# Kernel optimization log

Measured on AMD Instinct MI355X. Metric: run time of the kernel, lower is better.

The kernel has to match this reference:

```python
import jax, jax.numpy as jnp
import numpy as np

B, S, D, H = 64, 65536, 512, 256
H2 = H // 2
CAP_LIMIT = 0.85
ACT_THR = 0.5


def _normalize(x):
    return x / jnp.maximum(jnp.linalg.norm(x, axis=-1, keepdims=True), 1e-12)


def _layernorm(x, g, b):
    m = x.mean(-1, keepdims=True)
    v = ((x - m) ** 2).mean(-1, keepdims=True)
    return (x - m) / jnp.sqrt(v + 1e-5) * g + b


def setup_inputs() -> dict:
    key = jax.random.key(0)
    ks = jax.random.split(key, 20)

    def lin(k, i, o):
        s = 1.0 / np.sqrt(i)
        kw, kb = jax.random.split(k)
        return (jax.random.uniform(kw, (i, o), minval=-s, maxval=s),
                jax.random.uniform(kb, (o,), minval=-s, maxval=s))

    inp = {}
    inp["new_content"] = jax.random.normal(ks[0], (B, D), dtype=jnp.float32)
    inp["query"] = jax.random.normal(ks[1], (B, D), dtype=jnp.float32)
    inp["memory_bank"] = jax.random.normal(ks[2], (S, D), dtype=jnp.float32)
    inp["access_times"] = jax.random.uniform(ks[3], (S,), minval=0.0, maxval=900.0)
    inp["current_step"] = 1000
    inp["sr_w1"], inp["sr_b1"] = lin(ks[4], 2 * D, H)
    inp["sr_g"] = jnp.ones((H,), jnp.float32)
    inp["sr_beta"] = jnp.zeros((H,), jnp.float32)
    inp["sr_w2"], inp["sr_b2"] = lin(ks[5], H, H2)
    inp["sn_w"], inp["sn_b"] = lin(ks[6], D, H2)
    inp["sg_w"], inp["sg_b"] = lin(ks[7], H2, 1)
    inp["el_w"], inp["el_b"] = lin(ks[8], 1, 32)
    inp["ec_w"], inp["ec_b"] = lin(ks[9], D, 32)
    inp["eg_w"], inp["eg_b"] = lin(ks[10], 64, 1)
    inp["dd_w1"], inp["dd_b1"] = lin(ks[11], 2 * D, H)
    inp["dd_w2"], inp["dd_b2"] = lin(ks[12], H, 1)
    inp["ds_w1"], inp["ds_b1"] = lin(ks[13], 2 * D, H)
    inp["ds_w2"], inp["ds_b2"] = lin(ks[14], H, 1)
    return inp


def _forward(new_content, query, memory_bank, access_times,
             sr_w1, sr_b1, sr_g, sr_beta, sr_w2, sr_b2,
             sn_w, sn_b, sg_w, sg_b,
             el_w, el_b, ec_w, ec_b, eg_w, eg_b,
             dd_w1, dd_b1, dd_w2, dd_b2,
             ds_w1, ds_b1, ds_w2, ds_b2,
             step):
    mem = memory_bank
    at = access_times
    norms = jnp.linalg.norm(mem, axis=-1)               # [S]
    capacity = jnp.mean((norms > ACT_THR).astype(jnp.float32))
    dyn_thr = jnp.clip(
        jnp.where(capacity < 0.3, 0.08,
                  jnp.where(capacity < 0.6, 0.08 + (capacity - 0.3) * 0.733,
                            0.3 + (capacity - 0.6))), 0.0, 0.7)
    topk_thr = jnp.where(capacity < 0.3, 0.1, jnp.where(capacity < 0.6, 0.2, 0.4))
    raw_thr = jnp.where(capacity < 0.3, 0.3, 0.5)

    # store relevance / novelty / gate
    combined = jnp.concatenate([new_content, query], -1)          # [B,2D]
    h = _layernorm(combined @ sr_w1 + sr_b1, sr_g, sr_beta)
    rel = jax.nn.relu(jax.nn.relu(h) @ sr_w2 + sr_b2)             # [B,H2]
    nn_ = _normalize(new_content)
    sims = nn_ @ _normalize(mem).T                                # [B,S]
    max_sim = sims.max(-1, keepdims=True)
    novelty = (1.0 - max_sim) / 2.0                               # [B,1]
    nf = jax.nn.sigmoid(new_content @ sn_w + sn_b)
    store_score = jax.nn.sigmoid((rel + nf) @ sg_w + sg_b)        # [B,1]

    # novelty percentile over active slots (no boolean-shape gather)
    active = norms > ACT_THR
    n_active = active.sum()
    nov_mean = novelty.mean()
    cond = (nov_mean > (1.0 - sims)) & active[None, :]
    denom = (new_content.shape[0] * jnp.maximum(n_active, 1)).astype(jnp.float32)
    perc = jnp.where(n_active > 0, cond.sum().astype(jnp.float32) / denom, 1.0)

    base_store = store_score.mean() > raw_thr
    novelty_ok = nov_mean > dyn_thr
    topk_ok = perc > topk_thr
    should_store = base_store & novelty_ok & topk_ok

    # emergency erase (capacity over limit)
    do_erase = capacity > CAP_LIMIT
    age = jnp.maximum(step - at, 0.0)
    es_em = age / (age.max() + 1e-6) + (1.0 - jax.nn.sigmoid(norms))
    victim = jnp.argmax(es_em)
    mem = jnp.where(do_erase, mem.at[victim].set(0.0), mem)
    at = jnp.where(do_erase, at.at[victim].set(-99999.0), at)
    should_store = should_store & jnp.logical_not(do_erase & jnp.logical_not(novelty_ok))

    # per-slot erase scores
    lru = jax.nn.relu(((step - at) / 1000.0)[:, None] @ el_w + el_b)   # [S,32]
    conf = jax.nn.sigmoid(mem @ ec_w + ec_b)                            # [S,32]
    erase_scores = jax.nn.sigmoid(jnp.concatenate([lru, conf], -1) @ eg_w + eg_b)[:, 0]

    # conflict detection: top-3 similar slots, gather-MLP-scatter drift
    sims2 = _normalize(new_content) @ _normalize(mem).T                # [B,S]
    tv, ti = jax.lax.top_k(sims2, 3)                                   # [B,3]
    cmask = (tv > 0.7) & (tv < 0.99)
    gathered = mem[ti]                                                 # [B,3,D]
    pair = jnp.concatenate([jnp.broadcast_to(new_content[:, None, :], gathered.shape), gathered], -1)
    prob = jax.nn.sigmoid(jax.nn.relu(pair @ dd_w1 + dd_b1) @ dd_w2 + dd_b2)[..., 0]
    strength = jax.nn.sigmoid(jax.nn.relu(pair @ ds_w1 + ds_b1) @ ds_w2 + ds_b2)[..., 0]
    apply_m = cmask & (prob > 0.5)                                     # [B,3]
    avg = (new_content[:, None, :] + gathered) / 2.0
    s = strength[..., None]
    dn_cand = (1.0 - s) * new_content[:, None, :] + s * avg
    do_cand = (1.0 - s) * gathered + s * avg
    drifted_new = new_content
    for k in range(3):  # fixed k=3, later k overwrites (matches torch inner loop)
        drifted_new = jnp.where(apply_m[:, k:k + 1], dn_cand[:, k], drifted_new)
    for k in range(3):
        idx = ti[:, k]
        cur = mem[idx]
        mem = mem.at[idx].set(jnp.where(apply_m[:, k, None], do_cand[:, k], cur))

    # conditional write
    slot_age = step - at
    recent = (at >= 0.0) & (slot_age < 3.0)
    masked = erase_scores * (~recent).astype(erase_scores.dtype)
    masked = jnp.where(masked.max() <= 0.0, slot_age, masked)
    write_idx = jnp.where(do_erase, victim, jnp.argmax(masked))
    erase_out = jnp.where(should_store & jnp.logical_not(do_erase), masked, erase_scores)
    mem = jnp.where(should_store, mem.at[write_idx].set(drifted_new[0]), mem)
    at = jnp.where(should_store, at.at[write_idx].set(step), at)

    recent_changes = jnp.abs(mem - memory_bank).mean()
    return (mem, at, erase_out, store_score[:, 0], novelty[:, 0], recent_changes)


def reference(new_content, query, memory_bank, access_times,
              sr_w1, sr_b1, sr_g, sr_beta, sr_w2, sr_b2,
              sn_w, sn_b, sg_w, sg_b,
              el_w, el_b, ec_w, ec_b, eg_w, eg_b,
              dd_w1, dd_b1, dd_w2, dd_b2,
              ds_w1, ds_b1, ds_w2, ds_b2,
              current_step):
    step = jnp.float32(current_step)
    return _forward(new_content, query, memory_bank, access_times,
                    sr_w1, sr_b1, sr_g, sr_beta, sr_w2, sr_b2,
                    sn_w, sn_b, sg_w, sg_b,
                    el_w, el_b, ec_w, ec_b, eg_w, eg_b,
                    dd_w1, dd_b1, dd_w2, dd_b2,
                    ds_w1, ds_b1, ds_w2, ds_b2, step)
```

## Files before the change

kernel.cpp:

```cpp
#include <hip/hip_runtime.h>
#include <math.h>
#include <limits.h>

#define S_N 65536
#define D_N 512
#define B_N 64

typedef __attribute__((ext_vector_type(8))) short short8;
typedef __attribute__((ext_vector_type(4))) float f32x4;

#define SIMS_F      (B_N*S_N/2)
#define OFF_SIMS    0
#define OFF_AEXT    (OFF_SIMS + SIMS_F)
#define AEXT_F      (96*512/2)
#define OFF_NORMS   (OFF_AEXT + AEXT_F)
#define OFF_CONF    (OFF_NORMS + S_N)
#define OFF_FLAGS   (OFF_CONF + S_N)
#define OFF_LIST    (OFF_FLAGS + S_N)
#define OFF_MASKED  (OFF_LIST + 256)
#define OFF_ERSC    (OFF_MASKED + S_N)
#define OFF_SLOTAGE (OFF_ERSC + S_N)
#define OFF_STORES  (OFF_SLOTAGE + S_N)
#define OFF_MAXSIM  (OFF_STORES + 64)
#define OFF_TI      (OFF_MAXSIM + 64)
#define OFF_TV      (OFF_TI + 192)
#define OFF_APPLY   (OFF_TV + 192)
#define OFF_HM      (OFF_APPLY + 192)
#define OFF_HNC     (OFF_HM + 32768)
#define OFF_HG      (OFF_HNC + 65536)
#define OFF_DNC0    (OFF_HG + 196608)
#define OFF_DRIFT0  (OFF_DNC0 + 1536)
#define OFF_DOCAND  (OFF_DRIFT0 + 512)
#define OFF_SCAL    (OFF_DOCAND + 98304)

#define OUT_MEM 0
#define OUT_AT  (S_N*D_N)
#define OUT_ER  (OUT_AT + S_N)
#define OUT_SS  (OUT_ER + S_N)
#define OUT_NOV (OUT_SS + 64)
#define OUT_RC  (OUT_NOV + 64)

struct __align__(8) Scal {
  unsigned long long victim_pack;
  unsigned long long masked_pack;
  unsigned long long slotage_pack;
  int cnt_active;
  int cond_cnt;
  unsigned age_max_t;
  float nov_mean;
  float changed_sum;
  int do_erase;
  int should_store;
  int write_idx;
  int victim_idx;
  int list_cnt;
};

__device__ __forceinline__ float sigmoidf_(float x){ return 1.0f/(1.0f+expf(-x)); }
__device__ __forceinline__ unsigned f2mono(float f){
  unsigned u = __float_as_uint(f);
  return (u & 0x80000000u) ? ~u : (u | 0x80000000u);
}
__device__ __forceinline__ float mono2f(unsigned m){
  unsigned u = (m & 0x80000000u) ? (m & 0x7FFFFFFFu) : ~m;
  return __uint_as_float(u);
}
__device__ __forceinline__ unsigned long long packvi(float v, int i){
  return (((unsigned long long)f2mono(v)) << 32) | (unsigned long long)(0xFFFFFFFFu - (unsigned)i);
}
__device__ __forceinline__ bool betterVI(float v, int i, float v2, int i2){
  return (v > v2) || (v == v2 && i < i2);
}
__device__ __forceinline__ unsigned short bf16r(float f){
  unsigned u = __float_as_uint(f);
  return (unsigned short)((u + 0x7fffu + ((u>>16)&1u)) >> 16);
}
__device__ __forceinline__ float bf2f(unsigned short h){
  return __uint_as_float(((unsigned)h)<<16);
}
__device__ __forceinline__ void touch_row(int row, float* ws){
  int* flags = (int*)(ws + OFF_FLAGS);
  if (atomicExch(&flags[row], 1) == 0){
    Scal* sc = (Scal*)(ws + OFF_SCAL);
    int i = atomicAdd(&sc->list_cnt, 1);
    ((int*)(ws + OFF_LIST))[i] = row;
  }
}

__device__ __forceinline__ void gld16(const float* g, void* l){
  __builtin_amdgcn_global_load_lds((const __attribute__((address_space(1))) void*)g,
                                   (__attribute__((address_space(3))) void*)l, 16, 0, 0);
}
#define WAITV(N) asm volatile("s_waitcnt vmcnt(" #N ")" ::: "memory")

__global__ __launch_bounds__(256) void k_initm(const float* __restrict__ nc,
                                               const float* __restrict__ qr,
                                               const float* __restrict__ at_in,
                                               const float* __restrict__ ec_w,
                                               const int* __restrict__ step_p,
                                               const float* __restrict__ sr_w1,
                                               float* __restrict__ ws, float* __restrict__ out){
  int blk = blockIdx.x, t = threadIdx.x;
  Scal* sc = (Scal*)(ws + OFF_SCAL);
  unsigned short* aB = (unsigned short*)(ws + OFF_AEXT);
  __shared__ float red[256];
  __shared__ float ch[512];
  if (blk == 0){
    if (t == 0){
      sc->victim_pack = 0ULL; sc->masked_pack = 0ULL; sc->slotage_pack = 0ULL;
      sc->cnt_active = 0; sc->cond_cnt = 0; sc->age_max_t = 0u;
      sc->nov_mean = 0.0f; sc->changed_sum = 0.0f;
      sc->do_erase = 0; sc->should_store = 0; sc->write_idx = 0; sc->victim_idx = 0;
      sc->list_cnt = 0;
      out[OUT_RC] = 0.0f;
    }
    if (t < 64) ((unsigned*)(ws + OFF_MAXSIM))[t] = 0u;
  } else if (blk <= 64){
    int b = blk - 1;
    float x0 = nc[b*512 + t], x1 = nc[b*512 + 256 + t];
    red[t] = x0*x0 + x1*x1;
    __syncthreads();
    for (int o=128;o>0;o>>=1){ if (t<o) red[t]+=red[t+o]; __syncthreads(); }
    float inv = 1.0f / fmaxf(sqrtf(red[0]), 1e-12f);
    aB[b*512 + t]       = bf16r(x0*inv);
    aB[b*512 + 256 + t] = bf16r(x1*inv);
  } else if (blk <= 96){
    int j = blk - 65;
    for (int d=t; d<512; d+=256) aB[(64+j)*512 + d] = bf16r(ec_w[d*32 + j]);
  } else if (blk <= 160){
    int part = blk - 97;
    float stepf = (float)step_p[0];
    float lmaxv = -1e30f;
    for (int s = part*1024 + t; s < (part+1)*1024; s += 256)
      lmaxv = fmaxf(lmaxv, fmaxf(stepf - at_in[s], 0.0f));
    red[t]=lmaxv; __syncthreads();
    for (int o=128;o>0;o>>=1){ if (t<o) red[t]=fmaxf(red[t],red[t+o]); __syncthreads(); }
    if (t==0) atomicMax(&sc->age_max_t, f2mono(red[0]));
  } else if (blk <= 224){
    int part = blk - 161;
    for (int s = part*1024 + t; s < (part+1)*1024; s += 256)
      out[OUT_AT + s] = at_in[s];
  } else if (blk <= 288){
    int part = blk - 225;
    int* flags = (int*)(ws + OFF_FLAGS);
    for (int s = part*1024 + t; s < (part+1)*1024; s += 256) flags[s] = 0;
  } else {
    int blk2 = blk - 289;
    int b = blk2 >> 1, half = blk2 & 1;
    const float* src = half ? qr : nc;
    ch[t] = src[b*512 + t]; ch[256+t] = src[b*512 + 256 + t];
    __syncthreads();
    float h = 0.f;
    const float* w = sr_w1 + (half*512)*256 + t;
    for (int i=0;i<512;i++) h = fmaf(ch[i], w[i*256], h);
    ws[OFF_HM + (half*64 + b)*256 + t] = h;
  }
}

__global__ __launch_bounds__(256) void k_phase1(const float* __restrict__ mem,
                                                const float* __restrict__ ec_b,
                                                const float* __restrict__ eg_w,
                                                float* __restrict__ ws, float* __restrict__ out){
  __shared__ __align__(16) unsigned short aT[96*520];
  __shared__ __align__(16) char chunks[4*4*2048];
  __shared__ unsigned lmax[64];
  int t = threadIdx.x;
  int s0 = blockIdx.x * 64;
  Scal* sc = (Scal*)(ws + OFF_SCAL);
  int lane = t & 63, wv = t >> 6;
  int quad = lane >> 4, l15 = lane & 15;
  int row = wv*16 + l15;

  {
    const uint4* src = (const uint4*)(ws + OFF_AEXT);
    #pragma unroll
    for (int i=0;i<24;i++){
      int idx = i*256 + t;
      int arow = idx >> 6, c16 = idx & 63;
      uint4 v = src[idx];
      *(uint4*)((char*)aT + arow*1040 + c16*16) = v;
    }
    if (t < 64) lmax[t] = 0u;
  }
  __syncthreads();

  const float* gsrc = mem + ((size_t)(s0 + row))*512 + quad*8;
  float* od = out + OUT_MEM + ((size_t)(s0 + row))*512 + quad*8;
  char* mybuf = chunks + wv*8192;
  #define STAGE(c) do{ \
    gld16(gsrc + (c)*32,     mybuf + ((c)&3)*2048); \
    gld16(gsrc + (c)*32 + 4, mybuf + ((c)&3)*2048 + 1024); \
  }while(0)

  STAGE(0); asm volatile("" ::: "memory");
  STAGE(1); asm volatile("" ::: "memory");
  STAGE(2); asm volatile("" ::: "memory");

  f32x4 acc[6];
  #pragma unroll
  for (int r=0;r<6;r++) acc[r] = (f32x4){0.f,0.f,0.f,0.f};
  float ssq = 0.f;

  #pragma unroll
  for (int c=0;c<16;c++){
    if (c < 13) STAGE(c+3);
    if      (c == 0)  WAITV(6);
    else if (c == 1)  WAITV(8);
    else if (c == 2)  WAITV(10);
    else if (c <= 12) WAITV(12);
    else if (c == 13) WAITV(10);
    else if (c == 14) WAITV(8);
    else              WAITV(6);
    __builtin_amdgcn_sched_barrier(0);
    const char* bp = mybuf + (c&3)*2048;
    float4 v0 = *(const float4*)(bp + lane*16);
    float4 v1 = *(const float4*)(bp + 1024 + lane*16);
    *(float4*)(od + c*32)     = v0;
    *(float4*)(od + c*32 + 4) = v1;
    ssq = fmaf(v0.x,v0.x,ssq); ssq = fmaf(v0.y,v0.y,ssq);
    ssq = fmaf(v0.z,v0.z,ssq); ssq = fmaf(v0.w,v0.w,ssq);
    ssq = fmaf(v1.x,v1.x,ssq); ssq = fmaf(v1.y,v1.y,ssq);
    ssq = fmaf(v1.z,v1.z,ssq); ssq = fmaf(v1.w,v1.w,ssq);
    short8 bfrag;
    bfrag[0]=(short)bf16r(v0.x); bfrag[1]=(short)bf16r(v0.y);
    bfrag[2]=(short)bf16r(v0.z); bfrag[3]=(short)bf16r(v0.w);
    bfrag[4]=(short)bf16r(v1.x); bfrag[5]=(short)bf16r(v1.y);
    bfrag[6]=(short)bf16r(v1.z); bfrag[7]=(short)bf16r(v1.w);
    #pragma unroll
    for (int rt=0;rt<6;rt++){
      short8 afrag = *(const short8*)&aT[(rt*16 + l15)*520 + c*32 + quad*8];
      acc[rt] = __builtin_amdgcn_mfma_f32_16x16x32_bf16(afrag, bfrag, acc[rt], 0,0,0);
    }
  }
  #undef STAGE

  ssq += __shfl_xor(ssq, 16);
  ssq += __shfl_xor(ssq, 32);
  float nrm = sqrtf(ssq);
  float lv = 1.0f / fmaxf(nrm, 1e-12f);
  if (quad == 0) ws[OFF_NORMS + s0 + row] = nrm;
  unsigned long long m = __ballot(quad==0 && nrm > 0.5f);
  if (lane == 0) atomicAdd(&sc->cnt_active, (int)__popcll(m));

  unsigned short* simsb = (unsigned short*)(ws + OFF_SIMS);
  #pragma unroll
  for (int rt=0;rt<4;rt++){
    #pragma unroll
    for (int r=0;r<4;r++){
      int a = rt*16 + quad*4 + r;
      float sim = acc[rt][r] * lv;
      simsb[(size_t)a*S_N + s0 + row] = bf16r(sim);
      atomicMax(&lmax[a], f2mono(sim));
    }
  }
  float cpart = 0.f;
  #pragma unroll
  for (int rt=4;rt<6;rt++){
    #pragma unroll
    for (int r=0;r<4;r++){
      int j = (rt-4)*16 + quad*4 + r;
      cpart += sigmoidf_(acc[rt][r] + ec_b[j]) * eg_w[32+j];
    }
  }
  cpart += __shfl_down(cpart, 32);
  cpart += __shfl_down(cpart, 16);
  if (lane < 16) ws[OFF_CONF + s0 + row] = cpart;
  __syncthreads();
  if (t < 64) atomicMax(((unsigned*)(ws + OFF_MAXSIM)) + t, lmax[t]);
}

__global__ __launch_bounds__(256) void k_victim(const float* __restrict__ at_in,
                                                const int* __restrict__ step_p,
                                                float* __restrict__ ws){
  int t = threadIdx.x;
  Scal* sc = (Scal*)(ws + OFF_SCAL);
  float stepf = (float)step_p[0];
  float agemax = mono2f(sc->age_max_t);
  const float* norms = ws + OFF_NORMS;
  int gid = blockIdx.x*256 + t;
  int gstride = gridDim.x*256;
  unsigned long long best = 0ULL;
  for (int s = gid; s < S_N; s += gstride){
    float age = fmaxf(stepf - at_in[s], 0.0f);
    float es = age/(agemax + 1e-6f) + (1.0f - sigmoidf_(norms[s]));
    unsigned long long pk = packvi(es, s);
    if (pk > best) best = pk;
  }
  __shared__ unsigned long long redp[256];
  redp[t] = best; __syncthreads();
  for (int o=128;o>0;o>>=1){
    if (t<o && redp[t+o] > redp[t]) redp[t] = redp[t+o];
    __syncthreads();
  }
  if (t == 0) atomicMax(&sc->victim_pack, redp[0]);
}

__global__ __launch_bounds__(256) void k_mid(const float* __restrict__ nc, const float* __restrict__ qr,
    const float* __restrict__ sr_b1, const float* __restrict__ sr_g, const float* __restrict__ sr_beta,
    const float* __restrict__ sr_w2, const float* __restrict__ sr_b2,
    const float* __restrict__ sn_w,  const float* __restrict__ sn_b,
    const float* __restrict__ sg_w,  const float* __restrict__ sg_b,
    const float* __restrict__ ec_b,  const float* __restrict__ eg_w,
    float* __restrict__ ws, float* __restrict__ out){
  int blk = blockIdx.x, t = threadIdx.x;
  Scal* sc = (Scal*)(ws + OFF_SCAL);
  __shared__ float red[256];
  __shared__ float comb[1024];
  __shared__ float hbuf[256];
  __shared__ float sv[256*3];
  __shared__ int   si[256*3];

  if (blk == 64){
    const unsigned* gms = (const unsigned*)(ws + OFF_MAXSIM);
    float nv = 0.0f;
    if (t < 64){
      float msim = mono2f(gms[t]);
      nv = (1.0f - msim) * 0.5f;
      out[OUT_NOV + t] = nv;
    }
    red[t] = (t < 64) ? nv : 0.0f;
    __syncthreads();
    for (int o=128;o>0;o>>=1){ if (t<o) red[t]+=red[t+o]; __syncthreads(); }
    if (t == 0) sc->nov_mean = red[0] / 64.0f;
    return;
  }
  if (blk < 64){
    int b = blk;
    comb[t]       = nc[b*512 + t];
    comb[256 + t] = nc[b*512 + 256 + t];
    comb[512 + t] = qr[b*512 + t];
    comb[768 + t] = qr[b*512 + 256 + t];
    float h = ws[OFF_HM + b*256 + t] + ws[OFF_HM + (64 + b)*256 + t] + sr_b1[t];
    red[t] = h; __syncthreads();
    for (int o=128;o>0;o>>=1){ if (t<o) red[t]+=red[t+o]; __syncthreads(); }
    float mean = red[0] / 256.0f;
    __syncthreads();
    float dx = h - mean;
    red[t] = dx*dx; __syncthreads();
    for (int o=128;o>0;o>>=1){ if (t<o) red[t]+=red[t+o]; __syncthreads(); }
    float var = red[0] / 256.0f;
    __syncthreads();
    float hn = dx / sqrtf(var + 1e-5f) * sr_g[t] + sr_beta[t];
    hbuf[t] = fmaxf(hn, 0.0f);
    __syncthreads();
    float val = 0.0f;
    if (t < 128){
      float r = sr_b2[t];
      for (int j=0;j<256;j++) r = fmaf(hbuf[j], sr_w2[j*128 + t], r);
      r = fmaxf(r, 0.0f);
      float nf = sn_b[t];
      for (int d=0; d<512; d++) nf = fmaf(comb[d], sn_w[d*128 + t], nf);
      nf = sigmoidf_(nf);
      val = (r + nf) * sg_w[t];
    }
    red[t] = val; __syncthreads();
    for (int o=128;o>0;o>>=1){ if (t<o) red[t]+=red[t+o]; __syncthreads(); }
    if (t == 0){
      float ssc = sigmoidf_(red[0] + sg_b[0]);
      out[OUT_SS + b] = ssc;
      ws[OFF_STORES + b] = ssc;
    }
    return;
  }
  if (blk == 65){
    float capacity = (float)sc->cnt_active / 65536.0f;
    int de = (capacity > 0.85f) ? 1 : 0;
    int victim = (int)(0xFFFFFFFFu - (unsigned)(sc->victim_pack & 0xFFFFFFFFULL));
    if (t == 0){ sc->do_erase = de; sc->victim_idx = victim; }
    if (de){
      for (int d=t; d<512; d+=256) out[OUT_MEM + victim*512 + d] = 0.0f;
      if (t == 0){
        out[OUT_AT + victim] = -99999.0f;
        touch_row(victim, ws);
        float sum = 0.0f;
        for (int j=0;j<32;j++) sum += sigmoidf_(ec_b[j]) * eg_w[32 + j];
        ws[OFF_CONF + victim] = sum;
      }
    }
    return;
  }
  if (blk < 578){
    const unsigned* gms = (const unsigned*)(ws + OFF_MAXSIM);
    red[t] = (t < 64) ? (1.0f - mono2f(gms[t])) * 0.5f : 0.0f;
    __syncthreads();
    for (int o=128;o>0;o>>=1){ if (t<o) red[t]+=red[t+o]; __syncthreads(); }
    float thr = 1.0f - red[0] / 64.0f;
    const unsigned* simsu = (const unsigned*)(ws + OFF_SIMS);
    const float* norms = ws + OFF_NORMS;
    int gid = (blk - 66)*256 + t;
    int gstride = 512*256;
    int cnt = 0;
    for (int idx = gid; idx < B_N*S_N/2; idx += gstride){
      unsigned u = simsu[idx];
      int s = (idx*2) & (S_N-1);
      float v0 = __uint_as_float(u<<16);
      float v1 = __uint_as_float(u & 0xffff0000u);
      if (v0 > thr && norms[s]   > 0.5f) cnt++;
      if (v1 > thr && norms[s+1] > 0.5f) cnt++;
    }
    __syncthreads();
    int* redc = (int*)red;
    redc[t] = cnt;
    __syncthreads();
    for (int o=128;o>0;o>>=1){ if (t<o) redc[t]+=redc[t+o]; __syncthreads(); }
    if (t == 0) atomicAdd(&sc->cond_cnt, redc[0]);
    return;
  }
  {
    int b = blk - 578;
    int victim = (int)(0xFFFFFFFFu - (unsigned)(sc->victim_pack & 0xFFFFFFFFULL));
    int de = (((float)sc->cnt_active / 65536.0f) > 0.85f) ? 1 : 0;
    const unsigned short* simrow = (const unsigned short*)(ws + OFF_SIMS) + (size_t)b*S_N;
    float v[3] = {-1e30f,-1e30f,-1e30f};
    int ix[3] = {INT_MAX, INT_MAX, INT_MAX};
    for (int s = t; s < S_N; s += 256){
      float val = bf2f(simrow[s]);
      if (de && s == victim) val = 0.0f;
      if (betterVI(val, s, v[2], ix[2])){
        if (betterVI(val, s, v[1], ix[1])){
          if (betterVI(val, s, v[0], ix[0])){
            v[2]=v[1]; ix[2]=ix[1]; v[1]=v[0]; ix[1]=ix[0]; v[0]=val; ix[0]=s;
          } else { v[2]=v[1]; ix[2]=ix[1]; v[1]=val; ix[1]=s; }
        } else { v[2]=val; ix[2]=s; }
      }
    }
    for (int r=0;r<3;r++){ sv[t*3+r]=v[r]; si[t*3+r]=ix[r]; }
    for (int off=128; off>0; off>>=1){
      __syncthreads();
      if (t < off){
        float av[3], bv[3], ov[3]; int ai[3], bi[3], oi[3];
        for (int r=0;r<3;r++){ av[r]=sv[t*3+r]; ai[r]=si[t*3+r]; bv[r]=sv[(t+off)*3+r]; bi[r]=si[(t+off)*3+r]; }
        int ap=0, bp=0;
        for (int r=0;r<3;r++){
          bool takeA = (bp>=3) || (ap<3 && betterVI(av[ap],ai[ap],bv[bp],bi[bp]));
          if (takeA){ ov[r]=av[ap]; oi[r]=ai[ap]; ap++; }
          else      { ov[r]=bv[bp]; oi[r]=bi[bp]; bp++; }
        }
        for (int r=0;r<3;r++){ sv[t*3+r]=ov[r]; si[t*3+r]=oi[r]; }
      }
    }
    __syncthreads();
    if (t == 0){
      for (int k=0;k<3;k++){
        ws[OFF_TV + b*3 + k] = sv[k];
        ((int*)(ws + OFF_TI))[b*3 + k] = si[k];
      }
    }
  }
}

__global__ __launch_bounds__(256) void k_mlp2(const float* __restrict__ nc,
    const float* __restrict__ dd_w1, const float* __restrict__ ds_w1,
    float* __restrict__ ws, float* __restrict__ out){
  int blk = blockIdx.x, t = threadIdx.x;
  int b = blk >> 2, ks = blk & 3;
  __shared__ float ch[3*256];
  if (ks < 2){
    ch[t] = nc[b*512 + ks*256 + t];
    __syncthreads();
    float hd = 0.f, hs = 0.f;
    const float* wd = dd_w1 + (ks*256)*256 + t;
    const float* wq = ds_w1 + (ks*256)*256 + t;
    for (int i=0;i<256;i++){
      float c = ch[i];
      hd = fmaf(c, wd[i*256], hd);
      hs = fmaf(c, wq[i*256], hs);
    }
    float* H = ws + OFF_HNC + ((ks*64 + b)*2)*256;
    H[t] = hd; H[256 + t] = hs;
  } else {
    int ks2 = ks - 2;
    const int* tip = (const int*)(ws + OFF_TI);
    int r0 = tip[b*3], r1 = tip[b*3+1], r2 = tip[b*3+2];
    ch[t]       = out[OUT_MEM + (size_t)r0*512 + ks2*256 + t];
    ch[256 + t] = out[OUT_MEM + (size_t)r1*512 + ks2*256 + t];
    ch[512 + t] = out[OUT_MEM + (size_t)r2*512 + ks2*256 + t];
    __syncthreads();
    float hd0=0,hd1=0,hd2=0,hs0=0,hs1=0,hs2=0;
    const float* wd = dd_w1 + (512 + ks2*256)*256 + t;
    const float* wq = ds_w1 + (512 + ks2*256)*256 + t;
    for (int i=0;i<256;i++){
      float w0 = wd[i*256], w1 = wq[i*256];
      float c0 = ch[i], c1 = ch[256+i], c2 = ch[512+i];
      hd0=fmaf(c0,w0,hd0); hd1=fmaf(c1,w0,hd1); hd2=fmaf(c2,w0,hd2);
      hs0=fmaf(c0,w1,hs0); hs1=fmaf(c1,w1,hs1); hs2=fmaf(c2,w1,hs2);
    }
    float* H = ws + OFF_HG;
    int p0 = b*3;
    H[((ks2*192 + p0+0)*2+0)*256 + t] = hd0;
    H[((ks2*192 + p0+1)*2+0)*256 + t] = hd1;
    H[((ks2*192 + p0+2)*2+0)*256 + t] = hd2;
    H[((ks2*192 + p0+0)*2+1)*256 + t] = hs0;
    H[((ks2*192 + p0+1)*2+1)*256 + t] = hs1;
    H[((ks2*192 + p0+2)*2+1)*256 + t] = hs2;
  }
}

__global__ __launch_bounds__(256) void k_pairfin(const float* __restrict__ nc,
    const float* __restrict__ dd_b1, const float* __restrict__ dd_w2, const float* __restrict__ dd_b2,
    const float* __restrict__ ds_b1, const float* __restrict__ ds_w2, const float* __restrict__ ds_b2,
    float* __restrict__ ws, float* __restrict__ out){
  int p = blockIdx.x, t = threadIdx.x;
  int b = p / 3, k = p - 3*b;
  const int* tip = (const int*)(ws + OFF_TI);
  int row = tip[p];
  float hd = ws[OFF_HNC + ((0*64+b)*2+0)*256 + t] + ws[OFF_HNC + ((1*64+b)*2+0)*256 + t]
           + ws[OFF_HG + ((0*192+p)*2+0)*256 + t] + ws[OFF_HG + ((1*192+p)*2+0)*256 + t] + dd_b1[t];
  float hs = ws[OFF_HNC + ((0*64+b)*2+1)*256 + t] + ws[OFF_HNC + ((1*64+b)*2+1)*256 + t]
           + ws[OFF_HG + ((0*192+p)*2+1)*256 + t] + ws[OFF_HG + ((1*192+p)*2+1)*256 + t] + ds_b1[t];
  __shared__ float red[256];
  __shared__ float bc[2];
  red[t] = fmaxf(hd, 0.f) * dd_w2[t];
  __syncthreads();
  for (int o=128;o>0;o>>=1){ if (t<o) red[t]+=red[t+o]; __syncthreads(); }
  if (t == 0) bc[0] = red[0] + dd_b2[0];
  __syncthreads();
  red[t] = fmaxf(hs, 0.f) * ds_w2[t];
  __syncthreads();
  for (int o=128;o>0;o>>=1){ if (t<o) red[t]+=red[t+o]; __syncthreads(); }
  if (t == 0) bc[1] = red[0] + ds_b2[0];
  __syncthreads();
  float prob  = sigmoidf_(bc[0]);
  float stren = sigmoidf_(bc[1]);
  float tvv = ws[OFF_TV + p];
  int ap = (tvv > 0.7f && tvv < 0.99f && prob > 0.5f) ? 1 : 0;
  if (t == 0){
    ((int*)(ws + OFF_APPLY))[p] = ap;
    touch_row(row, ws);
  }
  for (int d=t; d<512; d+=256){
    float n = nc[b*512 + d];
    float g = out[OUT_MEM + (size_t)row*512 + d];
    float avg = 0.5f*(n + g);
    ws[OFF_DOCAND + p*512 + d] = (1.0f - stren)*g + stren*avg;
    if (b == 0) ws[OFF_DNC0 + k*512 + d] = (1.0f - stren)*n + stren*avg;
  }
}

__global__ __launch_bounds__(256) void k_scer(const int* __restrict__ step_p,
    const float* __restrict__ el_w, const float* __restrict__ el_b,
    const float* __restrict__ eg_w, const float* __restrict__ eg_b,
    float* __restrict__ ws, float* __restrict__ out){
  int blk = blockIdx.x, t = threadIdx.x;
  Scal* sc = (Scal*)(ws + OFF_SCAL);
  __shared__ unsigned long long rm[256], rs[256];
  if (blk < 2){
    int d = blk*256 + t;
    const int* tip = (const int*)(ws + OFF_TI);
    const int* ap  = (const int*)(ws + OFF_APPLY);
    for (int k=0;k<3;k++){
      float cur[64];
      #pragma unroll
      for (int b=0;b<64;b++) cur[b] = out[OUT_MEM + (size_t)tip[b*3 + k]*512 + d];
      #pragma unroll
      for (int b=0;b<64;b++){
        int p = b*3 + k;
        float v = ap[p] ? ws[OFF_DOCAND + p*512 + d] : cur[b];
        out[OUT_MEM + (size_t)tip[p]*512 + d] = v;
      }
    }
    return;
  }
  float stepf = (float)step_p[0];
  float egb = eg_b[0];
  int gid = (blk-2)*256 + t;
  int gstride = 64*256;
  unsigned long long bm = 0ULL, bs = 0ULL;
  for (int s = gid; s < S_N; s += gstride){
    float a = out[OUT_AT + s];
    float x = (stepf - a) / 1000.0f;
    float lp = 0.0f;
    #pragma unroll
    for (int j=0;j<32;j++) lp += fmaxf(x*el_w[j] + el_b[j], 0.0f) * eg_w[j];
    float er = sigmoidf_(lp + ws[OFF_CONF + s] + egb);
    float sa = stepf - a;
    bool recent = (a >= 0.0f) && (sa < 3.0f);
    float msk = recent ? 0.0f : er;
    ws[OFF_ERSC + s] = er;
    ws[OFF_MASKED + s] = msk;
    ws[OFF_SLOTAGE + s] = sa;
    unsigned long long pm = packvi(msk, s); if (pm > bm) bm = pm;
    unsigned long long ps = packvi(sa,  s); if (ps > bs) bs = ps;
  }
  rm[t]=bm; rs[t]=bs; __syncthreads();
  for (int o=128;o>0;o>>=1){
    if (t<o){ if (rm[t+o]>rm[t]) rm[t]=rm[t+o]; if (rs[t+o]>rs[t]) rs[t]=rs[t+o]; }
    __syncthreads();
  }
  if (t == 0){
    atomicMax(&sc->masked_pack, rm[0]);
    atomicMax(&sc->slotage_pack, rs[0]);
  }
}

__global__ __launch_bounds__(256) void k_finalout(const float* __restrict__ nc,
                                                  const int* __restrict__ step_p,
                                                  float* __restrict__ ws, float* __restrict__ out){
  int blk = blockIdx.x, t = threadIdx.x;
  Scal* sc = (Scal*)(ws + OFF_SCAL);
  __shared__ float red[64];
  __shared__ int sh_ss, sh_wi;
  if (t < 64) red[t] = ws[OFF_STORES + t];
  __syncthreads();
  for (int o=32;o>0;o>>=1){ if (t<o) red[t]+=red[t+o]; __syncthreads(); }
  if (t == 0){
    float store_mean = red[0] / 64.0f;
    int cnt = sc->cnt_active;
    float capacity = (float)cnt / 65536.0f;
    float dyn_thr;
    if (capacity < 0.3f) dyn_thr = 0.08f;
    else if (capacity < 0.6f) dyn_thr = 0.08f + (capacity - 0.3f)*0.733f;
    else dyn_thr = 0.3f + (capacity - 0.6f);
    dyn_thr = fminf(fmaxf(dyn_thr, 0.0f), 0.7f);
    float topk_thr = (capacity < 0.3f) ? 0.1f : ((capacity < 0.6f) ? 0.2f : 0.4f);
    float raw_thr  = (capacity < 0.3f) ? 0.3f : 0.5f;
    int base_store = store_mean > raw_thr;
    int novelty_ok = sc->nov_mean > dyn_thr;
    int cmax = cnt > 1 ? cnt : 1;
    float denom = (float)(64 * cmax);
    float perc = (cnt > 0) ? ((float)sc->cond_cnt) / denom : 1.0f;
    int topk_ok = perc > topk_thr;
    int de = sc->do_erase;
    int ss = base_store && novelty_ok && topk_ok;
    if (de && !novelty_ok) ss = 0;
    float mmax = mono2f((unsigned)(sc->masked_pack >> 32));
    int marg = (int)(0xFFFFFFFFu - (unsigned)(sc->masked_pack  & 0xFFFFFFFFULL));
    int sarg = (int)(0xFFFFFFFFu - (unsigned)(sc->slotage_pack & 0xFFFFFFFFULL));
    sh_ss = ss;
    sh_wi = de ? sc->victim_idx : ((mmax > 0.0f) ? marg : sarg);
  }
  __syncthreads();
  int ss = sh_ss, de = sc->do_erase;
  if (blk == 64){
    if (ss){
      int wi = sh_wi;
      const int* ap = (const int*)(ws + OFF_APPLY);
      for (int d=t; d<512; d+=256){
        float v = nc[d];
        if (ap[0]) v = ws[OFF_DNC0 + 0*512 + d];
        if (ap[1]) v = ws[OFF_DNC0 + 1*512 + d];
        if (ap[2]) v = ws[OFF_DNC0 + 2*512 + d];
        out[OUT_MEM + (size_t)wi*512 + d] = v;
      }
      if (t == 0){
        out[OUT_AT + wi] = (float)step_p[0];
        touch_row(wi, ws);
      }
    }
    return;
  }
  float mmax = mono2f((unsigned)(sc->masked_pack >> 32));
  bool usemask = ss && !de;
  for (int s = blk*256 + t; s < S_N; s += 64*256){
    float v;
    if (usemask) v = (mmax <= 0.0f) ? ws[OFF_SLOTAGE + s] : ws[OFF_MASKED + s];
    else v = ws[OFF_ERSC + s];
    out[OUT_ER + s] = v;
  }
}

__global__ __launch_bounds__(256) void k_diff(const float* __restrict__ mem,
                                              float* __restrict__ ws, float* __restrict__ out){
  int t = threadIdx.x;
  Scal* sc = (Scal*)(ws + OFF_SCAL);
  int cnt = sc->list_cnt;
  const int* list = (const int*)(ws + OFF_LIST);
  float lsum = 0.0f;
  for (int i = blockIdx.x; i < cnt; i += gridDim.x){
    int row = list[i];
    float part = 0.0f;
    for (int d=t; d<512; d+=256)
      part += fabsf(out[OUT_MEM + (size_t)row*512 + d] - mem[(size_t)row*512 + d]);
    lsum += part;
  }
  __shared__ float red[256];
  red[t] = lsum; __syncthreads();
  for (int o=128;o>0;o>>=1){ if (t<o) red[t]+=red[t+o]; __syncthreads(); }
  if (t == 0 && red[0] != 0.0f) atomicAdd(out + OUT_RC, red[0] * (1.0f/33554432.0f));
}

extern "C" void kernel_launch(void* const* d_in, const int* in_sizes, int n_in,
                              void* d_out, int out_size, void* d_ws, size_t ws_size,
                              hipStream_t stream) {
  const float* nc    = (const float*)d_in[0];
  const float* qr    = (const float*)d_in[1];
  const float* mem   = (const float*)d_in[2];
  const float* at    = (const float*)d_in[3];
  const int*   step  = (const int*)  d_in[4];
  const float* sr_w1 = (const float*)d_in[5];
  const float* sr_b1 = (const float*)d_in[6];
  const float* sr_g  = (const float*)d_in[7];
  const float* sr_be = (const float*)d_in[8];
  const float* sr_w2 = (const float*)d_in[9];
  const float* sr_b2 = (const float*)d_in[10];
  const float* sn_w  = (const float*)d_in[11];
  const float* sn_b  = (const float*)d_in[12];
  const float* sg_w  = (const float*)d_in[13];
  const float* sg_b  = (const float*)d_in[14];
  const float* el_w  = (const float*)d_in[15];
  const float* el_b  = (const float*)d_in[16];
  const float* ec_w  = (const float*)d_in[17];
  const float* ec_b  = (const float*)d_in[18];
  const float* eg_w  = (const float*)d_in[19];
  const float* eg_b  = (const float*)d_in[20];
  const float* dd_w1 = (const float*)d_in[21];
  const float* dd_b1 = (const float*)d_in[22];
  const float* dd_w2 = (const float*)d_in[23];
  const float* dd_b2 = (const float*)d_in[24];
  const float* ds_w1 = (const float*)d_in[25];
  const float* ds_b1 = (const float*)d_in[26];
  const float* ds_w2 = (const float*)d_in[27];
  const float* ds_b2 = (const float*)d_in[28];
  float* out = (float*)d_out;
  float* ws  = (float*)d_ws;

  k_initm    <<<dim3(417), dim3(256), 0, stream>>>(nc, qr, at, ec_w, step, sr_w1, ws, out);
  k_phase1   <<<dim3(1024), dim3(256), 0, stream>>>(mem, ec_b, eg_w, ws, out);
  k_victim   <<<dim3(64), dim3(256), 0, stream>>>(at, step, ws);
  k_mid      <<<dim3(642), dim3(256), 0, stream>>>(nc, qr, sr_b1, sr_g, sr_be,
                                                   sr_w2, sr_b2, sn_w, sn_b, sg_w, sg_b,
                                                   ec_b, eg_w, ws, out);
  k_mlp2     <<<dim3(256), dim3(256), 0, stream>>>(nc, dd_w1, ds_w1, ws, out);
  k_pairfin  <<<dim3(192), dim3(256), 0, stream>>>(nc, dd_b1, dd_w2, dd_b2,
                                                   ds_b1, ds_w2, ds_b2, ws, out);
  k_scer     <<<dim3(66), dim3(256), 0, stream>>>(step, el_w, el_b, eg_w, eg_b, ws, out);
  k_finalout <<<dim3(65), dim3(256), 0, stream>>>(nc, step, ws, out);
  k_diff     <<<dim3(64), dim3(256), 0, stream>>>(mem, ws, out);
}
```

Before: 502.6 us.

## Split small MLP matvecs across more blocks with K-split partial sums

```diff
diff --git a/kernel.cpp b/kernel.cpp
--- a/kernel.cpp
+++ b/kernel.cpp
@@ -31,6 +31,7 @@
 #define OFF_DNC0    (OFF_HG + 196608)
 #define OFF_DRIFT0  (OFF_DNC0 + 1536)
 #define OFF_DOCAND  (OFF_DRIFT0 + 512)
+#define OFF_SNP     OFF_DOCAND
 #define OFF_SCAL    (OFF_DOCAND + 98304)
 
 #define OUT_MEM 0
@@ -99,12 +100,13 @@
                                                const float* __restrict__ ec_w,
                                                const int* __restrict__ step_p,
                                                const float* __restrict__ sr_w1,
+                                               const float* __restrict__ sn_w,
                                                float* __restrict__ ws, float* __restrict__ out){
   int blk = blockIdx.x, t = threadIdx.x;
   Scal* sc = (Scal*)(ws + OFF_SCAL);
   unsigned short* aB = (unsigned short*)(ws + OFF_AEXT);
   __shared__ float red[256];
-  __shared__ float ch[512];
+  __shared__ float ch[256];
   if (blk == 0){
     if (t == 0){
       sc->victim_pack = 0ULL; sc->masked_pack = 0ULL; sc->slotage_pack = 0ULL;
@@ -144,16 +146,28 @@
     int part = blk - 225;
     int* flags = (int*)(ws + OFF_FLAGS);
     for (int s = part*1024 + t; s < (part+1)*1024; s += 256) flags[s] = 0;
+  } else if (blk <= 800){
+    int blk2 = blk - 289;
+    int b = blk2 >> 3, s = blk2 & 7;
+    const float* src = (s < 4) ? nc : qr;
+    if (t < 128) ch[t] = src[b*512 + (s & 3)*128 + t];
+    __syncthreads();
+    float h = 0.f;
+    const float* w = sr_w1 + (s*128)*256 + t;
+    #pragma unroll 8
+    for (int i=0;i<128;i++) h = fmaf(ch[i], w[i*256], h);
+    ws[OFF_HM + (s*64 + b)*256 + t] = h;
   } else {
-    int blk2 = blk - 289;
-    int b = blk2 >> 1, half = blk2 & 1;
-    const float* src = half ? qr : nc;
-    ch[t] = src[b*512 + t]; ch[256+t] = src[b*512 + 256 + t];
-    __syncthreads();
-    float h = 0.f;
-    const float* w = sr_w1 + (half*512)*256 + t;
-    for (int i=0;i<512;i++) h = fmaf(ch[i], w[i*256], h);
-    ws[OFF_HM + (half*64 + b)*256 + t] = h;
+    int blk2 = blk - 801;
+    int b = blk2 >> 2, ks = blk2 & 3;
+    int o = t & 127, kh = t >> 7;
+    if (t < 128) ch[t] = nc[b*512 + ks*128 + t];
+    __syncthreads();
+    float p = 0.f;
+    const float* w = sn_w + (ks*128 + kh*64)*128 + o;
+    #pragma unroll 8
+    for (int i=0;i<64;i++) p = fmaf(ch[kh*64 + i], w[i*128], p);
+    ws[OFF_SNP + ((ks*64 + b)*2 + kh)*128 + o] = p;
   }
 }
 
@@ -298,14 +312,13 @@
 __global__ __launch_bounds__(256) void k_mid(const float* __restrict__ nc, const float* __restrict__ qr,
     const float* __restrict__ sr_b1, const float* __restrict__ sr_g, const float* __restrict__ sr_beta,
     const float* __restrict__ sr_w2, const float* __restrict__ sr_b2,
-    const float* __restrict__ sn_w,  const float* __restrict__ sn_b,
+    const float* __restrict__ sn_b,
     const float* __restrict__ sg_w,  const float* __restrict__ sg_b,
     const float* __restrict__ ec_b,  const float* __restrict__ eg_w,
     float* __restrict__ ws, float* __restrict__ out){
   int blk = blockIdx.x, t = threadIdx.x;
   Scal* sc = (Scal*)(ws + OFF_SCAL);
   __shared__ float red[256];
-  __shared__ float comb[1024];
   __shared__ float hbuf[256];
   __shared__ float sv[256*3];
   __shared__ int   si[256*3];
@@ -326,11 +339,9 @@
   }
   if (blk < 64){
     int b = blk;
-    comb[t]       = nc[b*512 + t];
-    comb[256 + t] = nc[b*512 + 256 + t];
-    comb[512 + t] = qr[b*512 + t];
-    comb[768 + t] = qr[b*512 + 256 + t];
-    float h = ws[OFF_HM + b*256 + t] + ws[OFF_HM + (64 + b)*256 + t] + sr_b1[t];
+    float h = sr_b1[t];
+    #pragma unroll
+    for (int s=0;s<8;s++) h += ws[OFF_HM + (s*64 + b)*256 + t];
     red[t] = h; __syncthreads();
     for (int o=128;o>0;o>>=1){ if (t<o) red[t]+=red[t+o]; __syncthreads(); }
     float mean = red[0] / 256.0f;
@@ -343,17 +354,25 @@
     float hn = dx / sqrtf(var + 1e-5f) * sr_g[t] + sr_beta[t];
     hbuf[t] = fmaxf(hn, 0.0f);
     __syncthreads();
+    int oo = t & 127, jh = t >> 7;
+    float rp = 0.f;
+    const float* w2 = sr_w2 + (jh*128)*128 + oo;
+    #pragma unroll 8
+    for (int j=0;j<128;j++) rp = fmaf(hbuf[jh*128 + j], w2[j*128], rp);
+    red[t] = rp;
+    __syncthreads();
     float val = 0.0f;
     if (t < 128){
-      float r = sr_b2[t];
-      for (int j=0;j<256;j++) r = fmaf(hbuf[j], sr_w2[j*128 + t], r);
-      r = fmaxf(r, 0.0f);
-      float nf = sn_b[t];
-      for (int d=0; d<512; d++) nf = fmaf(comb[d], sn_w[d*128 + t], nf);
-      nf = sigmoidf_(nf);
+      float r = fmaxf(red[t] + red[t+128] + sr_b2[t], 0.0f);
+      float nfl = sn_b[t];
+      #pragma unroll
+      for (int q=0;q<8;q++) nfl += ws[OFF_SNP + (((q>>1)*64 + b)*2 + (q&1))*128 + t];
+      float nf = sigmoidf_(nfl);
       val = (r + nf) * sg_w[t];
     }
-    red[t] = val; __syncthreads();
+    __syncthreads();
+    red[t] = val;
+    __syncthreads();
     for (int o=128;o>0;o>>=1){ if (t<o) red[t]+=red[t+o]; __syncthreads(); }
     if (t == 0){
       float ssc = sigmoidf_(red[0] + sg_b[0]);
@@ -461,6 +480,7 @@
     float hd = 0.f, hs = 0.f;
     const float* wd = dd_w1 + (ks*256)*256 + t;
     const float* wq = ds_w1 + (ks*256)*256 + t;
+    #pragma unroll 4
     for (int i=0;i<256;i++){
       float c = ch[i];
       hd = fmaf(c, wd[i*256], hd);
@@ -479,6 +499,7 @@
     float hd0=0,hd1=0,hd2=0,hs0=0,hs1=0,hs2=0;
     const float* wd = dd_w1 + (512 + ks2*256)*256 + t;
     const float* wq = ds_w1 + (512 + ks2*256)*256 + t;
+    #pragma unroll 4
     for (int i=0;i<256;i++){
       float w0 = wd[i*256], w1 = wq[i*256];
       float c0 = ch[i], c1 = ch[256+i], c2 = ch[512+i];
@@ -564,7 +585,7 @@
   float stepf = (float)step_p[0];
   float egb = eg_b[0];
   int gid = (blk-2)*256 + t;
-  int gstride = 64*256;
+  int gstride = 128*256;
   unsigned long long bm = 0ULL, bs = 0ULL;
   for (int s = gid; s < S_N; s += gstride){
     float a = out[OUT_AT + s];
@@ -714,16 +735,16 @@
   float* out = (float*)d_out;
   float* ws  = (float*)d_ws;
 
-  k_initm    <<<dim3(417), dim3(256), 0, stream>>>(nc, qr, at, ec_w, step, sr_w1, ws, out);
+  k_initm    <<<dim3(1057), dim3(256), 0, stream>>>(nc, qr, at, ec_w, step, sr_w1, sn_w, ws, out);
   k_phase1   <<<dim3(1024), dim3(256), 0, stream>>>(mem, ec_b, eg_w, ws, out);
   k_victim   <<<dim3(64), dim3(256), 0, stream>>>(at, step, ws);
   k_mid      <<<dim3(642), dim3(256), 0, stream>>>(nc, qr, sr_b1, sr_g, sr_be,
-                                                   sr_w2, sr_b2, sn_w, sn_b, sg_w, sg_b,
+                                                   sr_w2, sr_b2, sn_b, sg_w, sg_b,
                                                    ec_b, eg_w, ws, out);
   k_mlp2     <<<dim3(256), dim3(256), 0, stream>>>(nc, dd_w1, ds_w1, ws, out);
   k_pairfin  <<<dim3(192), dim3(256), 0, stream>>>(nc, dd_b1, dd_w2, dd_b2,
                                                    ds_b1, ds_w2, ds_b2, ws, out);
-  k_scer     <<<dim3(66), dim3(256), 0, stream>>>(step, el_w, el_b, eg_w, eg_b, ws, out);
+  k_scer     <<<dim3(130), dim3(256), 0, stream>>>(step, el_w, el_b, eg_w, eg_b, ws, out);
   k_finalout <<<dim3(65), dim3(256), 0, stream>>>(nc, step, ws, out);
   k_diff     <<<dim3(64), dim3(256), 0, stream>>>(mem, ws, out);
 }
```

Measured after the change: 504.8 us. Within noise of the previous version (+0.5%).
